# Kernel optimization log

Hardware: AMD Instinct MI355X
Metric: run time of the kernel (lower is better)

The kernel has to match this reference:

```python
import jax, jax.numpy as jnp
import numpy as np

NA, NM = 200000, 100000
DA, DM = 128, 64
H = 128
E = 1000000


def _lin(x, W, b):
    # torch nn.Linear: y = x @ W.T + b, W: [out, in]
    return x @ W.T + b


def setup_inputs() -> dict:
    key = jax.random.key(0)
    ks = jax.random.split(key, 24)
    s = 0.02
    inp = {
        "x_account": jax.random.normal(ks[0], (NA, DA), jnp.float32),
        "x_merchant": jax.random.normal(ks[1], (NM, DM), jnp.float32),
        "e_am_src": jax.random.randint(ks[2], (E,), 0, NA, jnp.int32),
        "e_am_dst": jax.random.randint(ks[3], (E,), 0, NM, jnp.int32),
        "e_am_w": jax.random.uniform(ks[4], (E,), jnp.float32),
        "e_ma_src": jax.random.randint(ks[5], (E,), 0, NM, jnp.int32),
        "e_ma_dst": jax.random.randint(ks[6], (E,), 0, NA, jnp.int32),
        "e_ma_w": jax.random.uniform(ks[7], (E,), jnp.float32),
        # type_proj
        "Wp_a": s * jax.random.normal(ks[8], (H, DA), jnp.float32),
        "bp_a": jnp.zeros((H,), jnp.float32),
        "Wp_m": s * jax.random.normal(ks[9], (H, DM), jnp.float32),
        "bp_m": jnp.zeros((H,), jnp.float32),
        # rel_linears: account->merchant:txn (in=DA), merchant->account:rev (in=DM)
        "Wr_am": s * jax.random.normal(ks[10], (H, DA), jnp.float32),
        "br_am": jnp.zeros((H,), jnp.float32),
        "Wr_ma": s * jax.random.normal(ks[11], (H, DM), jnp.float32),
        "br_ma": jnp.zeros((H,), jnp.float32),
        # combine MLPs (Linear(2H,H) + ReLU)
        "Wc_a": s * jax.random.normal(ks[12], (H, 2 * H), jnp.float32),
        "bc_a": jnp.zeros((H,), jnp.float32),
        "Wc_m": s * jax.random.normal(ks[13], (H, 2 * H), jnp.float32),
        "bc_m": jnp.zeros((H,), jnp.float32),
        # account_out
        "Wo": s * jax.random.normal(ks[14], (1, H), jnp.float32),
        "bo": jnp.zeros((1,), jnp.float32),
    }
    return inp


def reference(x_account, x_merchant, e_am_src, e_am_dst, e_am_w,
              e_ma_src, e_ma_dst, e_ma_w,
              Wp_a, bp_a, Wp_m, bp_m,
              Wr_am, br_am, Wr_ma, br_ma,
              Wc_a, bc_a, Wc_m, bc_m, Wo, bo):
    # self projection per node type
    proj_a = _lin(x_account, Wp_a, bp_a)   # [NA, H]
    proj_m = _lin(x_merchant, Wp_m, bp_m)  # [NM, H]

    # relation account->merchant: lin(src feats) then SpMM (weighted scatter-add to dst)
    lin_am = _lin(x_account, Wr_am, br_am)                    # [NA, H]
    msg_am = e_am_w[:, None] * lin_am[e_am_src]               # [E, H]
    neigh_m = jax.ops.segment_sum(msg_am, e_am_dst, num_segments=proj_m.shape[0])

    # relation merchant->account
    lin_ma = _lin(x_merchant, Wr_ma, br_ma)                   # [NM, H]
    msg_ma = e_ma_w[:, None] * lin_ma[e_ma_src]               # [E, H]
    neigh_a = jax.ops.segment_sum(msg_ma, e_ma_dst, num_segments=proj_a.shape[0])

    # concat + MLP combine per node type
    h_a = jax.nn.relu(_lin(jnp.concatenate([proj_a, neigh_a], axis=1), Wc_a, bc_a))
    h_m = jax.nn.relu(_lin(jnp.concatenate([proj_m, neigh_m], axis=1), Wc_m, bc_m))
    _ = h_m  # computed in original but only account head is returned

    acct_out = jax.nn.sigmoid(_lin(h_a, Wo, bo))[:, 0]        # [NA]
    return acct_out
```

## Files before the change

kernel.cpp:

```cpp
#include <hip/hip_runtime.h>


typedef __attribute__((ext_vector_type(8))) short short8;
typedef __attribute__((ext_vector_type(4))) float f32x4;

__device__ inline unsigned short f32_bf16(float f) {
  unsigned int u = __float_as_uint(f);
  u += 0x7FFF + ((u >> 16) & 1);
  return (unsigned short)(u >> 16);
}
__device__ inline unsigned int pk_bf16(float a, float b) {
  return (unsigned int)f32_bf16(a) | ((unsigned int)f32_bf16(b) << 16);
}

__global__ void fence0_kernel(const float* __restrict__ xa, float* __restrict__ probe) {
  int lane = threadIdx.x & 63;
  probe[lane] = xa[lane] * 0.5f;
}

__global__ void cvt_xm_kernel(const float* __restrict__ xm,
                              unsigned int* __restrict__ xmbf, int npairs) {
  int i = blockIdx.x * 256 + threadIdx.x;
  if (i < npairs) {
    float2 v = ((const float2*)xm)[i];
    xmbf[i] = pk_bf16(v.x, v.y);
  }
}

__global__ __launch_bounds__(256) void prep_kernel(
    const float* __restrict__ Wp_a, const float* __restrict__ bp_a,
    const float* __restrict__ Wr_ma, const float* __restrict__ br_ma,
    const float* __restrict__ Wc_a, const float* __restrict__ bc_a,
    unsigned short* __restrict__ Wcomb, float* __restrict__ beff,
    float* __restrict__ vbr) {
  __shared__ float wc_s[256];
  int col = blockIdx.x;
  int t = threadIdx.x;
  wc_s[t] = Wc_a[col * 256 + t];
  __syncthreads();
  int wave = t >> 6, lane = t & 63;
  if (wave < 2) {
    int k = t;
    float acc = 0.f;
#pragma unroll
    for (int j = 0; j < 128; j += 4) {
      float a0 = Wp_a[(j + 0) * 128 + k];
      float a1 = Wp_a[(j + 1) * 128 + k];
      float a2 = Wp_a[(j + 2) * 128 + k];
      float a3 = Wp_a[(j + 3) * 128 + k];
      acc += wc_s[j] * a0 + wc_s[j + 1] * a1 + wc_s[j + 2] * a2 + wc_s[j + 3] * a3;
    }
    Wcomb[col * 192 + k] = f32_bf16(acc);
  } else if (wave == 2) {
    int kk = lane;
    float acc = 0.f;
#pragma unroll
    for (int j = 0; j < 128; j += 4) {
      float a0 = Wr_ma[(j + 0) * 64 + kk];
      float a1 = Wr_ma[(j + 1) * 64 + kk];
      float a2 = Wr_ma[(j + 2) * 64 + kk];
      float a3 = Wr_ma[(j + 3) * 64 + kk];
      acc += wc_s[128 + j] * a0 + wc_s[129 + j] * a1 + wc_s[130 + j] * a2 + wc_s[131 + j] * a3;
    }
    Wcomb[col * 192 + 128 + kk] = f32_bf16(acc);
  } else {
    float v1 = wc_s[lane] * bp_a[lane] + wc_s[lane + 64] * bp_a[lane + 64];
    float v2 = wc_s[128 + lane] * br_ma[lane] + wc_s[192 + lane] * br_ma[lane + 64];
#pragma unroll
    for (int m = 1; m <= 32; m <<= 1) {
      v1 += __shfl_xor(v1, m, 64);
      v2 += __shfl_xor(v2, m, 64);
    }
    if (lane == 0) { beff[col] = v1 + bc_a[col]; vbr[col] = v2; }
  }
}

__global__ void hist_kernel(const int* __restrict__ dst, int* __restrict__ counts, int E) {
  int e = blockIdx.x * 256 + threadIdx.x;
  if (e < E) atomicAdd(&counts[dst[e]], 1);
}

__global__ void scan_a(const int* __restrict__ counts, int* __restrict__ bsum, int NA) {
  __shared__ int tmp[256];
  int t = threadIdx.x;
  int i = blockIdx.x * 256 + t;
  tmp[t] = (i < NA) ? counts[i] : 0;
  __syncthreads();
  for (int off = 128; off > 0; off >>= 1) {
    if (t < off) tmp[t] += tmp[t + off];
    __syncthreads();
  }
  if (t == 0) bsum[blockIdx.x] = tmp[0];
}

__global__ void scan_b(const int* __restrict__ bsum, int* __restrict__ bexcl, int nb) {
  __shared__ int tmp[1024];
  int t = threadIdx.x;
  int v = (t < nb) ? bsum[t] : 0;
  tmp[t] = v;
  __syncthreads();
  for (int off = 1; off < 1024; off <<= 1) {
    int x = (t >= off) ? tmp[t - off] : 0;
    __syncthreads();
    tmp[t] += x;
    __syncthreads();
  }
  bexcl[t] = tmp[t] - v;
}

__global__ void scan_c(const int* __restrict__ counts, const int* __restrict__ bexcl,
                       int* __restrict__ rowstart, int* __restrict__ cursor, int NA) {
  __shared__ int tmp[256];
  int t = threadIdx.x;
  int i = blockIdx.x * 256 + t;
  int v = (i < NA) ? counts[i] : 0;
  tmp[t] = v;
  __syncthreads();
  for (int off = 1; off < 256; off <<= 1) {
    int x = (t >= off) ? tmp[t - off] : 0;
    __syncthreads();
    tmp[t] += x;
    __syncthreads();
  }
  int excl = bexcl[blockIdx.x] + tmp[t] - v;
  if (i < NA) { rowstart[i] = excl; cursor[i] = excl; }
  else if (i == NA) { rowstart[NA] = excl; }
}

__global__ void scatter_kernel(const int* __restrict__ src, const int* __restrict__ dst,
                               const float* __restrict__ w, int* __restrict__ cursor,
                               unsigned long long* __restrict__ edges, int E) {
  int e = blockIdx.x * 256 + threadIdx.x;
  if (e >= E) return;
  int d = dst[e];
  int pos = atomicAdd(&cursor[d], 1);
  unsigned long long pk = (unsigned int)src[e] |
                          ((unsigned long long)__float_as_uint(w[e]) << 32);
  edges[pos] = pk;
}

__global__ __launch_bounds__(256) void gather_kernel(
    const unsigned int* __restrict__ xmbf, const unsigned long long* __restrict__ edges,
    const int* __restrict__ rowstart, unsigned int* __restrict__ neighbf,
    float* __restrict__ sumw, int NA) {
  int wave = threadIdx.x >> 6, lane = threadIdx.x & 63;
  int a = blockIdx.x * 4 + wave;
  if (a >= NA) return;
  int half = lane >> 5;
  int fp = lane & 31;
  int s0 = rowstart[a], s1 = rowstart[a + 1];
  float accx = 0.f, accy = 0.f, ws = 0.f;
  for (int e0 = s0; e0 < s1; e0 += 8) {
#pragma unroll
    for (int k = 0; k < 4; ++k) {
      int e = e0 + k * 2 + half;
      bool valid = e < s1;
      unsigned long long p = edges[valid ? e : s0];
      float w = valid ? __uint_as_float((unsigned int)(p >> 32)) : 0.f;
      unsigned int s = (unsigned int)p;
      unsigned int xp = xmbf[(size_t)s * 32 + fp];
      float x0 = __uint_as_float(xp << 16);
      float x1 = __uint_as_float(xp & 0xffff0000u);
      accx += w * x0;
      accy += w * x1;
      ws += w;
    }
  }
  accx += __shfl_xor(accx, 32, 64);
  accy += __shfl_xor(accy, 32, 64);
  ws   += __shfl_xor(ws, 32, 64);
  if (half == 0) {
    neighbf[(size_t)a * 32 + fp] = pk_bf16(accx, accy);
    if (fp == 0) sumw[a] = ws;
  }
}

__global__ __launch_bounds__(256) void acct_kernel(
    const float* __restrict__ xa, const unsigned int* __restrict__ neighbf,
    const float* __restrict__ sumw, const unsigned int* __restrict__ Wcomb32,
    const float* __restrict__ beff, const float* __restrict__ vbr,
    const float* __restrict__ Wo, const float* __restrict__ bo,
    float* __restrict__ out, int NA) {
  __shared__ unsigned int B_lds[24 * 128 * 4];
  int tid = threadIdx.x;
#pragma unroll
  for (int it = 0; it < 12; ++it) {
    int i = tid + it * 256;
    int c = i >> 7, col = i & 127;
    uint4 v = ((const uint4*)Wcomb32)[col * 24 + c];
    *((uint4*)&B_lds[i * 4]) = v;
  }
  __syncthreads();

  int wave = tid >> 6, lane = tid & 63;
  int n15 = lane & 15, quad = lane >> 4;
  float bo0 = bo[0];

  union U4 { uint4 u; short8 h; };

#pragma unroll
  for (int tile = 0; tile < 2; ++tile) {
    int rowbase = blockIdx.x * 128 + (wave * 2 + tile) * 16;
    int m = rowbase + n15;
    int mc = min(m, NA - 1);

    U4 afr[6];
    const float* xrow = xa + (size_t)mc * 128 + quad * 8;
#pragma unroll
    for (int s = 0; s < 4; ++s) {
      float4 f0 = ((const float4*)(xrow + s * 32))[0];
      float4 f1 = ((const float4*)(xrow + s * 32))[1];
      afr[s].u = make_uint4(pk_bf16(f0.x, f0.y), pk_bf16(f0.z, f0.w),
                            pk_bf16(f1.x, f1.y), pk_bf16(f1.z, f1.w));
    }
#pragma unroll
    for (int s = 0; s < 2; ++s) {
      afr[4 + s].u = ((const uint4*)(neighbf + (size_t)mc * 32))[s * 4 + quad];
    }

    f32x4 acc[8];
#pragma unroll
    for (int t = 0; t < 8; ++t) acc[t] = (f32x4){0.f, 0.f, 0.f, 0.f};

#pragma unroll
    for (int s = 0; s < 6; ++s) {
#pragma unroll
      for (int t = 0; t < 8; ++t) {
        U4 bfr;
        bfr.u = *((const uint4*)&B_lds[((s * 4 + quad) * 128 + t * 16 + n15) * 4]);
        acc[t] = __builtin_amdgcn_mfma_f32_16x16x32_bf16(afr[s].h, bfr.h, acc[t], 0, 0, 0);
      }
    }

    float sw[4];
#pragma unroll
    for (int r = 0; r < 4; ++r) {
      int grow = rowbase + quad * 4 + r;
      sw[r] = (grow < NA) ? sumw[grow] : 0.f;
    }
    float rowsum[4] = {0.f, 0.f, 0.f, 0.f};
#pragma unroll
    for (int t = 0; t < 8; ++t) {
      int col = t * 16 + n15;
      float be = beff[col], vb = vbr[col], wo = Wo[col];
#pragma unroll
      for (int r = 0; r < 4; ++r) {
        float h = acc[t][r] + be + sw[r] * vb;
        h = fmaxf(h, 0.f);
        rowsum[r] += h * wo;
      }
    }
#pragma unroll
    for (int msk = 1; msk <= 8; msk <<= 1) {
#pragma unroll
      for (int r = 0; r < 4; ++r) rowsum[r] += __shfl_xor(rowsum[r], msk, 64);
    }
    if (n15 == 0) {
#pragma unroll
      for (int r = 0; r < 4; ++r) {
        int grow = rowbase + quad * 4 + r;
        if (grow < NA) out[grow] = 1.0f / (1.0f + __expf(-(rowsum[r] + bo0)));
      }
    }
  }
}

extern "C" void kernel_launch(void* const* d_in, const int* in_sizes, int n_in,
                              void* d_out, int out_size, void* d_ws, size_t ws_size,
                              hipStream_t stream) {
  const float* xa      = (const float*)d_in[0];
  const float* xm      = (const float*)d_in[1];
  const int*   ema_src = (const int*)d_in[5];
  const int*   ema_dst = (const int*)d_in[6];
  const float* ema_w   = (const float*)d_in[7];
  const float* Wp_a    = (const float*)d_in[8];
  const float* bp_a    = (const float*)d_in[9];
  const float* Wr_ma   = (const float*)d_in[14];
  const float* br_ma   = (const float*)d_in[15];
  const float* Wc_a    = (const float*)d_in[16];
  const float* bc_a    = (const float*)d_in[17];
  const float* Wo      = (const float*)d_in[20];
  const float* bo      = (const float*)d_in[21];

  int NA = in_sizes[0] / 128;
  int NM = in_sizes[1] / 64;
  int E  = in_sizes[5];

  char* ws = (char*)d_ws;
  size_t off = 0;
  auto take = [&](size_t bytes) { char* p = ws + off; off = (off + bytes + 255) & ~(size_t)255; return p; };
  unsigned int* neighbf = (unsigned int*)take((size_t)NA * 32 * 4);
  unsigned int* xmbf    = (unsigned int*)take((size_t)NM * 32 * 4);
  float* sumw           = (float*)take((size_t)NA * 4);
  int* counts           = (int*)take((size_t)NA * 4);
  int* rowstart         = (int*)take((size_t)(NA + 1) * 4);
  int* cursor           = (int*)take((size_t)NA * 4);
  int* bsum             = (int*)take(1024 * 4);
  int* bexcl            = (int*)take(1024 * 4);
  unsigned long long* edges = (unsigned long long*)take((size_t)E * 8);
  unsigned short* Wcomb = (unsigned short*)take(128 * 192 * 2);
  float* beff           = (float*)take(128 * 4);
  float* vbr            = (float*)take(128 * 4);
  float* probe          = (float*)take(64 * 4);

  fence0_kernel<<<1, 64, 0, stream>>>(xa, probe);

  hipMemsetAsync(counts, 0, (size_t)NA * 4, stream);

  int npairs = NM * 32;
  cvt_xm_kernel<<<(npairs + 255) / 256, 256, 0, stream>>>(xm, xmbf, npairs);

  int ebn = (E + 255) / 256;
  hist_kernel<<<ebn, 256, 0, stream>>>(ema_dst, counts, E);

  prep_kernel<<<128, 256, 0, stream>>>(Wp_a, bp_a, Wr_ma, br_ma, Wc_a, bc_a, Wcomb, beff, vbr);

  int nb = (NA + 256) / 256;
  scan_a<<<nb, 256, 0, stream>>>(counts, bsum, NA);
  scan_b<<<1, 1024, 0, stream>>>(bsum, bexcl, nb);
  scan_c<<<nb, 256, 0, stream>>>(counts, bexcl, rowstart, cursor, NA);

  scatter_kernel<<<ebn, 256, 0, stream>>>(ema_src, ema_dst, ema_w, cursor, edges, E);

  int gb = (NA + 3) / 4;
  gather_kernel<<<gb, 256, 0, stream>>>(xmbf, edges, rowstart, neighbf, sumw, NA);

  int ab = (NA + 127) / 128;
  acct_kernel<<<ab, 256, 0, stream>>>(xa, neighbf, sumw, (const unsigned int*)Wcomb,
                                      beff, vbr, Wo, bo, (float*)d_out, NA);
}
```

Baseline: 393.2 us.

## Bucket edges by 128-node destination blocks and accumulate in LDS with atomics

Replaces the per-node CSR (histogram over 200k nodes, a three-kernel scan, per-node gather) with coarse buckets of 128 destination nodes. Counting and the single-kernel scan now run over about 1.6k buckets. Each block accumulates its bucket's messages into a shared-memory tile using LDS float atomics, with the local destination packed into the edge record. This removes the large scan passes and the scatter's atomic contention on individual nodes. In exchange it adds LDS atomic traffic, a load imbalance that depends on bucket sizes, and a nondeterministic summation order.

```diff
diff --git a/kernel.cpp b/kernel.cpp
--- a/kernel.cpp
+++ b/kernel.cpp
@@ -3,6 +3,9 @@
 
 typedef __attribute__((ext_vector_type(8))) short short8;
 typedef __attribute__((ext_vector_type(4))) float f32x4;
+
+#define BK 128
+#define BSH 7
 
 __device__ inline unsigned short f32_bf16(float f) {
   unsigned int u = __float_as_uint(f);
@@ -77,54 +80,29 @@
 
 __global__ void hist_kernel(const int* __restrict__ dst, int* __restrict__ counts, int E) {
   int e = blockIdx.x * 256 + threadIdx.x;
-  if (e < E) atomicAdd(&counts[dst[e]], 1);
-}
-
-__global__ void scan_a(const int* __restrict__ counts, int* __restrict__ bsum, int NA) {
-  __shared__ int tmp[256];
+  if (e < E) atomicAdd(&counts[dst[e] >> BSH], 1);
+}
+
+__global__ __launch_bounds__(1024) void scan_kernel(
+    const int* __restrict__ counts, int* __restrict__ boff,
+    int* __restrict__ cursor, int NB) {
+  __shared__ int part[1024];
   int t = threadIdx.x;
-  int i = blockIdx.x * 256 + t;
-  tmp[t] = (i < NA) ? counts[i] : 0;
-  __syncthreads();
-  for (int off = 128; off > 0; off >>= 1) {
-    if (t < off) tmp[t] += tmp[t + off];
+  int i0 = 2 * t, i1 = 2 * t + 1;
+  int v0 = (i0 < NB) ? counts[i0] : 0;
+  int v1 = (i1 < NB) ? counts[i1] : 0;
+  int p = v0 + v1;
+  part[t] = p;
+  __syncthreads();
+  for (int off = 1; off < 1024; off <<= 1) {
+    int x = (t >= off) ? part[t - off] : 0;
     __syncthreads();
-  }
-  if (t == 0) bsum[blockIdx.x] = tmp[0];
-}
-
-__global__ void scan_b(const int* __restrict__ bsum, int* __restrict__ bexcl, int nb) {
-  __shared__ int tmp[1024];
-  int t = threadIdx.x;
-  int v = (t < nb) ? bsum[t] : 0;
-  tmp[t] = v;
-  __syncthreads();
-  for (int off = 1; off < 1024; off <<= 1) {
-    int x = (t >= off) ? tmp[t - off] : 0;
+    part[t] += x;
     __syncthreads();
-    tmp[t] += x;
-    __syncthreads();
-  }
-  bexcl[t] = tmp[t] - v;
-}
-
-__global__ void scan_c(const int* __restrict__ counts, const int* __restrict__ bexcl,
-                       int* __restrict__ rowstart, int* __restrict__ cursor, int NA) {
-  __shared__ int tmp[256];
-  int t = threadIdx.x;
-  int i = blockIdx.x * 256 + t;
-  int v = (i < NA) ? counts[i] : 0;
-  tmp[t] = v;
-  __syncthreads();
-  for (int off = 1; off < 256; off <<= 1) {
-    int x = (t >= off) ? tmp[t - off] : 0;
-    __syncthreads();
-    tmp[t] += x;
-    __syncthreads();
-  }
-  int excl = bexcl[blockIdx.x] + tmp[t] - v;
-  if (i < NA) { rowstart[i] = excl; cursor[i] = excl; }
-  else if (i == NA) { rowstart[NA] = excl; }
+  }
+  int excl = part[t] - p;
+  if (i0 <= NB) { boff[i0] = excl; cursor[i0] = excl; }
+  if (i1 <= NB) { boff[i1] = excl + v0; cursor[i1] = excl + v0; }
 }
 
 __global__ void scatter_kernel(const int* __restrict__ src, const int* __restrict__ dst,
@@ -133,45 +111,63 @@
   int e = blockIdx.x * 256 + threadIdx.x;
   if (e >= E) return;
   int d = dst[e];
-  int pos = atomicAdd(&cursor[d], 1);
-  unsigned long long pk = (unsigned int)src[e] |
-                          ((unsigned long long)__float_as_uint(w[e]) << 32);
+  int b = d >> BSH;
+  int pos = atomicAdd(&cursor[b], 1);
+  unsigned long long pk = ((unsigned long long)__float_as_uint(w[e]) << 32) |
+                          ((unsigned int)(d & (BK - 1)) << 24) | (unsigned int)src[e];
   edges[pos] = pk;
 }
 
-__global__ __launch_bounds__(256) void gather_kernel(
+__global__ __launch_bounds__(256) void accum_kernel(
     const unsigned int* __restrict__ xmbf, const unsigned long long* __restrict__ edges,
-    const int* __restrict__ rowstart, unsigned int* __restrict__ neighbf,
+    const int* __restrict__ boff, unsigned int* __restrict__ neighbf,
     float* __restrict__ sumw, int NA) {
-  int wave = threadIdx.x >> 6, lane = threadIdx.x & 63;
-  int a = blockIdx.x * 4 + wave;
-  if (a >= NA) return;
-  int half = lane >> 5;
-  int fp = lane & 31;
-  int s0 = rowstart[a], s1 = rowstart[a + 1];
-  float accx = 0.f, accy = 0.f, ws = 0.f;
-  for (int e0 = s0; e0 < s1; e0 += 8) {
+  __shared__ float acc[BK * 65];
+  int tid = threadIdx.x;
+  for (int i = tid; i < BK * 65; i += 256) acc[i] = 0.f;
+  __syncthreads();
+
+  int b = blockIdx.x;
+  int s0 = boff[b], s1 = boff[b + 1];
+  int wave = tid >> 6, lane = tid & 63;
+  int fp = lane >> 1, hi = lane & 1;
+
+  for (int e0 = s0 + wave * 4; e0 < s1; e0 += 16) {
+    unsigned long long rec[4];
+    unsigned int xp[4];
+    bool val[4];
 #pragma unroll
     for (int k = 0; k < 4; ++k) {
-      int e = e0 + k * 2 + half;
-      bool valid = e < s1;
-      unsigned long long p = edges[valid ? e : s0];
-      float w = valid ? __uint_as_float((unsigned int)(p >> 32)) : 0.f;
-      unsigned int s = (unsigned int)p;
-      unsigned int xp = xmbf[(size_t)s * 32 + fp];
-      float x0 = __uint_as_float(xp << 16);
-      float x1 = __uint_as_float(xp & 0xffff0000u);
-      accx += w * x0;
-      accy += w * x1;
-      ws += w;
-    }
-  }
-  accx += __shfl_xor(accx, 32, 64);
-  accy += __shfl_xor(accy, 32, 64);
-  ws   += __shfl_xor(ws, 32, 64);
-  if (half == 0) {
-    neighbf[(size_t)a * 32 + fp] = pk_bf16(accx, accy);
-    if (fp == 0) sumw[a] = ws;
+      int e = e0 + k;
+      val[k] = e < s1;
+      rec[k] = edges[val[k] ? e : s0];
+      xp[k] = xmbf[(size_t)(rec[k] & 0xffffffu) * 32 + fp];
+    }
+#pragma unroll
+    for (int k = 0; k < 4; ++k) {
+      if (val[k]) {
+        float w = __uint_as_float((unsigned int)(rec[k] >> 32));
+        float x = hi ? __uint_as_float(xp[k] & 0xffff0000u)
+                     : __uint_as_float(xp[k] << 16);
+        int dl = (int)((rec[k] >> 24) & (BK - 1));
+        atomicAdd(&acc[dl * 65 + lane], w * x);
+        if (lane == 0) atomicAdd(&acc[dl * 65 + 64], w);
+      }
+    }
+  }
+  __syncthreads();
+
+  int a0 = b * BK;
+  for (int i = tid; i < BK * 32; i += 256) {
+    int al = i >> 5, pp = i & 31;
+    int a = a0 + al;
+    if (a < NA)
+      neighbf[(size_t)a * 32 + pp] = pk_bf16(acc[al * 65 + 2 * pp],
+                                             acc[al * 65 + 2 * pp + 1]);
+  }
+  for (int i = tid; i < BK; i += 256) {
+    int a = a0 + i;
+    if (a < NA) sumw[a] = acc[i * 65 + 64];
   }
 }
 
@@ -285,6 +281,7 @@
   int NA = in_sizes[0] / 128;
   int NM = in_sizes[1] / 64;
   int E  = in_sizes[5];
+  int NB = (NA + BK - 1) / BK;
 
   char* ws = (char*)d_ws;
   size_t off = 0;
@@ -292,11 +289,9 @@
   unsigned int* neighbf = (unsigned int*)take((size_t)NA * 32 * 4);
   unsigned int* xmbf    = (unsigned int*)take((size_t)NM * 32 * 4);
   float* sumw           = (float*)take((size_t)NA * 4);
-  int* counts           = (int*)take((size_t)NA * 4);
-  int* rowstart         = (int*)take((size_t)(NA + 1) * 4);
-  int* cursor           = (int*)take((size_t)NA * 4);
-  int* bsum             = (int*)take(1024 * 4);
-  int* bexcl            = (int*)take(1024 * 4);
+  int* counts           = (int*)take((size_t)(NB + 2) * 4);
+  int* boff             = (int*)take((size_t)(NB + 2) * 4);
+  int* cursor           = (int*)take((size_t)(NB + 2) * 4);
   unsigned long long* edges = (unsigned long long*)take((size_t)E * 8);
   unsigned short* Wcomb = (unsigned short*)take(128 * 192 * 2);
   float* beff           = (float*)take(128 * 4);
@@ -305,25 +300,21 @@
 
   fence0_kernel<<<1, 64, 0, stream>>>(xa, probe);
 
-  hipMemsetAsync(counts, 0, (size_t)NA * 4, stream);
+  hipMemsetAsync(counts, 0, (size_t)(NB + 2) * 4, stream);
 
   int npairs = NM * 32;
   cvt_xm_kernel<<<(npairs + 255) / 256, 256, 0, stream>>>(xm, xmbf, npairs);
 
+  prep_kernel<<<128, 256, 0, stream>>>(Wp_a, bp_a, Wr_ma, br_ma, Wc_a, bc_a, Wcomb, beff, vbr);
+
   int ebn = (E + 255) / 256;
   hist_kernel<<<ebn, 256, 0, stream>>>(ema_dst, counts, E);
 
-  prep_kernel<<<128, 256, 0, stream>>>(Wp_a, bp_a, Wr_ma, br_ma, Wc_a, bc_a, Wcomb, beff, vbr);
-
-  int nb = (NA + 256) / 256;
-  scan_a<<<nb, 256, 0, stream>>>(counts, bsum, NA);
-  scan_b<<<1, 1024, 0, stream>>>(bsum, bexcl, nb);
-  scan_c<<<nb, 256, 0, stream>>>(counts, bexcl, rowstart, cursor, NA);
+  scan_kernel<<<1, 1024, 0, stream>>>(counts, boff, cursor, NB);
 
   scatter_kernel<<<ebn, 256, 0, stream>>>(ema_src, ema_dst, ema_w, cursor, edges, E);
 
-  int gb = (NA + 3) / 4;
-  gather_kernel<<<gb, 256, 0, stream>>>(xmbf, edges, rowstart, neighbf, sumw, NA);
+  accum_kernel<<<NB, 256, 0, stream>>>(xmbf, edges, boff, neighbf, sumw, NA);
 
   int ab = (NA + 127) / 128;
   acct_kernel<<<ab, 256, 0, stream>>>(xa, neighbf, sumw, (const unsigned int*)Wcomb,
```

Result: slower. 911.8 us (+131.9%).
